# Kernel tuning notes

Measured on AMD Instinct MI355X. Metric: run time of the kernel, lower is better.

The kernel has to match this reference:

```python
import jax, jax.numpy as jnp
import numpy as np

B, D, E, H, L = 16384, 512, 16, 256, 64
NOISE_EPS = 0.01


def setup_inputs() -> dict:
    key = jax.random.key(0)
    ks = jax.random.split(key, 8)
    s = 0.05
    return {
        "x": jax.random.normal(ks[0], (B, D), dtype=jnp.float32),
        "noise": jax.random.normal(ks[1], (B, E), dtype=jnp.float32),
        "w_gate": jax.random.normal(ks[2], (D, E), dtype=jnp.float32) * s,
        "w_noise": jax.random.normal(ks[3], (D, E), dtype=jnp.float32) * s,
        "W1": jax.random.normal(ks[4], (E, D, H), dtype=jnp.float32) * s,
        "b1": jnp.zeros((E, H), dtype=jnp.float32),
        "W2": jax.random.normal(ks[5], (E, H, L), dtype=jnp.float32) * s,
        "b2": jnp.zeros((E, L), dtype=jnp.float32),
    }


def _noisy_gating(x, noise, w_gate, w_noise):
    clean_logits = x @ w_gate                                   # [B, E]
    noise_stddev = jax.nn.softplus(x @ w_noise) + NOISE_EPS     # [B, E]
    logits = jax.nn.softmax(clean_logits + noise * noise_stddev, axis=1)
    mean_weight = jnp.mean(logits, axis=-1) - 1e-8              # [B]
    gates = jnp.where(logits >= mean_weight[:, None], logits, 0.0)
    gates = gates / jnp.sum(gates, axis=-1, keepdims=True)
    return gates


def reference(x, noise, w_gate, w_noise, W1, b1, W2, b2):
    gates = _noisy_gating(x, noise, w_gate, w_noise)            # [B, E]
    # Dense equivalent of SparseDispatcher dispatch -> expert MLP -> combine:
    # combine scatters expert_e(x[b]) * gates[b,e] into slot (b, e), zeros elsewhere;
    # since gates==0 at masked slots, this equals gates[:,:,None] * all-expert outputs.
    h = jnp.tanh(jnp.einsum("bd,edh->beh", x, W1) + b1[None])   # [B, E, H]
    y = jnp.einsum("beh,ehl->bel", h, W2) + b2[None]            # [B, E, L]
    return gates[:, :, None] * y                                # [B, E, L]
```

## Files before the change

### kernel.cpp

```cpp
#include <hip/hip_runtime.h>
#include <stdint.h>

#define BROWS 16384
#define DDIM  512
#define EEXP  16
#define HDIM  256
#define LDIM  64
#define BM    64

typedef __bf16  bf16x8  __attribute__((ext_vector_type(8)));
typedef float   floatx4 __attribute__((ext_vector_type(4)));
typedef ushort  ushort8 __attribute__((ext_vector_type(8)));
typedef unsigned int u32;

__device__ __forceinline__ ushort f2bf(float f) {
    uint32_t u = __builtin_bit_cast(uint32_t, f);
    u += 0x7fffu + ((u >> 16) & 1u);
    return (ushort)(u >> 16);
}

__device__ __forceinline__ float fast_tanh(float x) {
    float e = __builtin_amdgcn_exp2f(x * 2.8853900817779268f);
    return 1.0f - 2.0f * __builtin_amdgcn_rcpf(e + 1.0f);
}

__device__ __forceinline__ void gl_lds16(const void* g, void* l) {
    __builtin_amdgcn_global_load_lds(
        (const __attribute__((address_space(1))) u32*)g,
        (__attribute__((address_space(3))) u32*)l, 16, 0, 0);
}

__global__ __launch_bounds__(256) void gate_aux_kernel(
    const float* __restrict__ x,
    const float* __restrict__ noise,
    const float* __restrict__ wg,
    const float* __restrict__ wn,
    const float* __restrict__ W1,
    const float* __restrict__ W2,
    float* __restrict__ gates,
    ushort* __restrict__ xbf,
    ushort* __restrict__ W1T,
    ushort* __restrict__ W2T,
    u32* __restrict__ cnt,
    u32* __restrict__ rowlist,
    float* __restrict__ out)
{
    if (blockIdx.x >= 512) {
        __shared__ float tile[32][33];
        int b = blockIdx.x - 512;
        const float* src; ushort* dst; int R, C, c0, r0, swz, ei;
        if (b < 2048) {
            ei = b >> 7; int rem = b & 127;
            c0 = (rem & 7) * 32; r0 = (rem >> 3) * 32;
            R = DDIM; C = HDIM; swz = 1;
            src = W1; dst = W1T;
        } else {
            b -= 2048;
            ei = b >> 4; int rem = b & 15;
            c0 = (rem & 1) * 32; r0 = (rem >> 1) * 32;
            R = HDIM; C = LDIM; swz = 0;
            src = W2; dst = W2T;
        }
        const int tx = threadIdx.x & 31, ty = threadIdx.x >> 5;
        const float* s = src + (size_t)ei * R * C;
        ushort* d = dst + (size_t)ei * R * C;

        #pragma unroll
        for (int i = 0; i < 4; ++i) {
            int rr = ty + i * 8;
            tile[rr][tx] = s[(size_t)(r0 + rr) * C + c0 + tx];
        }
        __syncthreads();
        #pragma unroll
        for (int i = 0; i < 4; ++i) {
            int cc = ty + i * 8;
            int h = c0 + cc;
            int col = r0 + tx;
            int col2 = col;
            if (swz) {
                int g = (col >> 3) & 7;
                col2 = (col & ~63) | ((g ^ (h & 7)) << 3) | (col & 7);
            }
            d[(size_t)h * R + col2] = f2bf(tile[tx][cc]);
        }
        return;
    }

    __shared__ __align__(16) float xs[32 * 132];
    __shared__ __align__(16) float wTg[16 * 132];
    __shared__ __align__(16) float wTn[16 * 132];
    __shared__ u32 lcnt[16];
    __shared__ u32 lbase[16];
    __shared__ ushort lrows[16 * 32];

    const int t    = threadIdx.x;
    const int blk  = blockIdx.x;
    const int row0 = blk * 32;
    const int og   = t & 15, rg = t >> 4;

    if (t < 16) lcnt[t] = 0;

    floatx4 accg4[2] = {}, accn4[2] = {};

    for (int ch = 0; ch < 4; ++ch) {
        const int k0 = ch * 128;
        __syncthreads();
        {
            int r = t >> 3, c = (t & 7) * 16;
            const float* src = &x[(size_t)(row0 + r) * DDIM + k0 + c];
            float4 f[4];
            #pragma unroll
            for (int i = 0; i < 4; ++i)
                f[i] = reinterpret_cast<const float4*>(src)[i];
            float* dst = &xs[r * 132 + c];
            #pragma unroll
            for (int i = 0; i < 4; ++i)
                reinterpret_cast<float4*>(dst)[i] = f[i];

            const int row = row0 + r;
            const int sw  = r & 7;
            #pragma unroll
            for (int i = 0; i < 2; ++i) {
                int cb = k0 + c + i * 8;
                int kb = cb >> 6;
                int g  = (cb >> 3) & 7;
                int gp = g ^ sw;
                float4 a = f[i * 2], b = f[i * 2 + 1];
                ushort8 t8;
                t8[0]=f2bf(a.x); t8[1]=f2bf(a.y); t8[2]=f2bf(a.z); t8[3]=f2bf(a.w);
                t8[4]=f2bf(b.x); t8[5]=f2bf(b.y); t8[6]=f2bf(b.z); t8[7]=f2bf(b.w);
                *reinterpret_cast<ushort8*>(&xbf[(size_t)row * DDIM + kb * 64 + gp * 8]) = t8;
            }
        }
        {
            int d = t >> 1, e0 = (t & 1) * 8;
            float4 a0 = *reinterpret_cast<const float4*>(&wg[(size_t)(k0 + d) * EEXP + e0]);
            float4 a1 = *reinterpret_cast<const float4*>(&wg[(size_t)(k0 + d) * EEXP + e0 + 4]);
            float4 b0 = *reinterpret_cast<const float4*>(&wn[(size_t)(k0 + d) * EEXP + e0]);
            float4 b1 = *reinterpret_cast<const float4*>(&wn[(size_t)(k0 + d) * EEXP + e0 + 4]);
            wTg[(e0+0)*132+d]=a0.x; wTg[(e0+1)*132+d]=a0.y; wTg[(e0+2)*132+d]=a0.z; wTg[(e0+3)*132+d]=a0.w;
            wTg[(e0+4)*132+d]=a1.x; wTg[(e0+5)*132+d]=a1.y; wTg[(e0+6)*132+d]=a1.z; wTg[(e0+7)*132+d]=a1.w;
            wTn[(e0+0)*132+d]=b0.x; wTn[(e0+1)*132+d]=b0.y; wTn[(e0+2)*132+d]=b0.z; wTn[(e0+3)*132+d]=b0.w;
            wTn[(e0+4)*132+d]=b1.x; wTn[(e0+5)*132+d]=b1.y; wTn[(e0+6)*132+d]=b1.z; wTn[(e0+7)*132+d]=b1.w;
        }
        __syncthreads();

        #pragma unroll 8
        for (int d4 = 0; d4 < 32; ++d4) {
            floatx4 wgv = *reinterpret_cast<const floatx4*>(&wTg[og * 132 + d4 * 4]);
            floatx4 wnv = *reinterpret_cast<const floatx4*>(&wTn[og * 132 + d4 * 4]);
            #pragma unroll
            for (int rr = 0; rr < 2; ++rr) {
                floatx4 xv = *reinterpret_cast<const floatx4*>(&xs[(rg * 2 + rr) * 132 + d4 * 4]);
                accg4[rr] += xv * wgv;
                accn4[rr] += xv * wnv;
            }
        }
    }

    #pragma unroll
    for (int rr = 0; rr < 2; ++rr) {
        const int row = row0 + rg * 2 + rr;
        float accg = accg4[rr][0] + accg4[rr][1] + accg4[rr][2] + accg4[rr][3];
        float accn = accn4[rr][0] + accn4[rr][1] + accn4[rr][2] + accn4[rr][3];

        float sp = fmaxf(accn, 0.f) + log1pf(expf(-fabsf(accn)));
        float stddev = sp + 0.01f;
        float nz = noise[(size_t)row * EEXP + og];
        float z = accg + nz * stddev;

        float m = z;
        #pragma unroll
        for (int mask = 8; mask >= 1; mask >>= 1)
            m = fmaxf(m, __shfl_xor(m, mask, 16));
        float ez = expf(z - m);
        float s = ez;
        #pragma unroll
        for (int mask = 8; mask >= 1; mask >>= 1)
            s += __shfl_xor(s, mask, 16);
        float logit = ez / s;

        float lsum = logit;
        #pragma unroll
        for (int mask = 8; mask >= 1; mask >>= 1)
            lsum += __shfl_xor(lsum, mask, 16);
        float mean = lsum * (1.0f / 16.0f) - 1e-8f;

        float gate = (logit >= mean) ? logit : 0.0f;
        float denom = gate;
        #pragma unroll
        for (int mask = 8; mask >= 1; mask >>= 1)
            denom += __shfl_xor(denom, mask, 16);

        gates[(size_t)row * EEXP + og] = gate / denom;

        if (gate > 0.0f) {
            u32 p = atomicAdd(&lcnt[og], 1u);
            lrows[og * 32 + p] = (ushort)(rg * 2 + rr);
        } else {
            float4 zf = {0.f, 0.f, 0.f, 0.f};
            float4* o = reinterpret_cast<float4*>(
                &out[(size_t)row * (EEXP * LDIM) + og * LDIM]);
            #pragma unroll
            for (int i = 0; i < 16; ++i) o[i] = zf;
        }
    }

    __syncthreads();
    if (t < 16) lbase[t] = atomicAdd(&cnt[t], lcnt[t]);
    __syncthreads();
    for (int i = t; i < 16 * 32; i += 256) {
        int e = i >> 5, j = i & 31;
        if ((u32)j < lcnt[e])
            rowlist[(size_t)e * BROWS + lbase[e] + j] = row0 + lrows[e * 32 + j];
    }
}

__global__ __launch_bounds__(256, 4) void expert_kernel(
    const ushort* __restrict__ xbf,
    const float*  __restrict__ gates,
    const ushort* __restrict__ W1T,
    const float*  __restrict__ b1,
    const ushort* __restrict__ W2T,
    const float*  __restrict__ b2,
    const u32*    __restrict__ cnt,
    const u32*    __restrict__ rowlist,
    float* __restrict__ out)
{
    __shared__ __align__(16) ushort lds[20480];

    const int bx = blockIdx.x;
    const int e  = bx & 15;
    const int t  = bx >> 4;

    const int count = (int)cnt[e];
    if (t * BM >= count) return;
    const int nrt = min(BM, count - t * BM);
    const u32* rl = rowlist + (size_t)e * BROWS + t * BM;

    const int tid  = threadIdx.x;
    const int lane = tid & 63;
    const int wave = tid >> 6;

    const int lr = lane & 15;
    const int q  = lane >> 4;
    const int kq = q * 8;
    const int rq = q * 4;
    const int la = lane >> 3, lb = lane & 7;

    const char* xg = (const char*)xbf;
    const char* w1 = (const char*)W1T + (size_t)e * HDIM * 1024;

    size_t abase[2]; int sxr[2];
    #pragma unroll
    for (int p = 0; p < 2; ++p) {
        int r  = wave * 16 + p * 8 + la;
        int rc = min(r, nrt - 1);
        u32 ri = rl[rc];
        abase[p] = (size_t)ri * 1024;
        sxr[p]   = (la ^ (int)(ri & 7)) << 4;
    }

    floatx4 acc[4][4] = {};

    for (int kb = 0; kb < 8; ++kb) {
        const int koff = kb * 128;
        #pragma unroll
        for (int p = 0; p < 2; ++p) {
            int c = wave * 2 + p;
            gl_lds16(xg + abase[p] + koff + ((lb << 4) ^ sxr[p]), &lds[c * 512]);
        }
        #pragma unroll
        for (int p = 0; p < 8; ++p) {
            int c = wave * 8 + p;
            gl_lds16(w1 + (size_t)(c * 8 + la) * 1024 + koff + (lb << 4),
                     &lds[4096 + c * 512]);
        }
        __syncthreads();

        #pragma unroll
        for (int s = 0; s < 2; ++s) {
            const int g = s * 4 + q;
            bf16x8 af[4], bfr[4];
            #pragma unroll
            for (int i = 0; i < 4; ++i) {
                int r = i * 16 + lr;
                af[i] = *reinterpret_cast<const bf16x8*>(&lds[r * 64 + ((g ^ (r & 7)) << 3)]);
            }
            #pragma unroll
            for (int j = 0; j < 4; ++j) {
                int r = wave * 64 + j * 16 + lr;
                bfr[j] = *reinterpret_cast<const bf16x8*>(&lds[4096 + r * 64 + ((g ^ (r & 7)) << 3)]);
            }
            #pragma unroll
            for (int i = 0; i < 4; ++i)
                #pragma unroll
                for (int j = 0; j < 4; ++j)
                    acc[i][j] = __builtin_amdgcn_mfma_f32_16x16x32_bf16(
                        af[i], bfr[j], acc[i][j], 0, 0, 0);
        }
        __syncthreads();
    }

    float b1v[4];
    #pragma unroll
    for (int j = 0; j < 4; ++j)
        b1v[j] = b1[e * HDIM + wave * 64 + j * 16 + lr];

    #pragma unroll
    for (int i = 0; i < 4; ++i)
        #pragma unroll
        for (int j = 0; j < 4; ++j) {
            int c = wave * 64 + j * 16 + lr;
            int gg = c >> 3;
            #pragma unroll
            for (int rr = 0; rr < 4; ++rr) {
                int r = i * 16 + rq + rr;
                float v = fast_tanh(acc[i][j][rr] + b1v[j]);
                lds[r * 256 + (((gg & 24) | ((gg & 7) ^ (r & 7))) << 3) + (c & 7)] = f2bf(v);
            }
        }
    __syncthreads();

    const ushort* w2 = W2T + (size_t)e * LDIM * HDIM;
    floatx4 acc2[4] = {};
    #pragma unroll
    for (int s = 0; s < 8; ++s) {
        int r = wave * 16 + lr;
        int g = s * 4 + q;
        bf16x8 af = *reinterpret_cast<const bf16x8*>(
            &lds[r * 256 + (((g & 24) | ((g & 7) ^ (r & 7))) << 3)]);
        #pragma unroll
        for (int j = 0; j < 4; ++j) {
            bf16x8 bfr = *reinterpret_cast<const bf16x8*>(
                &w2[(size_t)(j * 16 + lr) * HDIM + s * 32 + kq]);
            acc2[j] = __builtin_amdgcn_mfma_f32_16x16x32_bf16(af, bfr, acc2[j], 0, 0, 0);
        }
    }

    float b2v[4];
    #pragma unroll
    for (int j = 0; j < 4; ++j)
        b2v[j] = b2[e * LDIM + j * 16 + lr];

    #pragma unroll
    for (int rr = 0; rr < 4; ++rr) {
        int r  = wave * 16 + rq + rr;
        int rc = min(r, nrt - 1);
        u32 ri = rl[rc];
        float gsc = gates[(size_t)ri * EEXP + e];
        if (r < nrt) {
            #pragma unroll
            for (int j = 0; j < 4; ++j)
                out[(size_t)ri * (EEXP * LDIM) + e * LDIM + j * 16 + lr] =
                    (acc2[j][rr] + b2v[j]) * gsc;
        }
    }
}

extern "C" void kernel_launch(void* const* d_in, const int* in_sizes, int n_in,
                              void* d_out, int out_size, void* d_ws, size_t ws_size,
                              hipStream_t stream) {
    (void)in_sizes; (void)n_in; (void)out_size; (void)ws_size;
    const float* x     = (const float*)d_in[0];
    const float* noise = (const float*)d_in[1];
    const float* wg    = (const float*)d_in[2];
    const float* wn    = (const float*)d_in[3];
    const float* W1    = (const float*)d_in[4];
    const float* b1    = (const float*)d_in[5];
    const float* W2    = (const float*)d_in[6];
    const float* b2    = (const float*)d_in[7];
    float* out = (float*)d_out;

    char* ws = (char*)d_ws;
    float*  gates   = (float*)ws;
    ushort* W1T     = (ushort*)(ws + (1 << 20));
    ushort* W2T     = (ushort*)(ws + (5 << 20));
    ushort* xbf     = (ushort*)(ws + (6 << 20));
    u32*    cnt     = (u32*)(ws + (22 << 20));
    u32*    rowlist = (u32*)(ws + (24 << 20));

    hipMemsetAsync(cnt, 0, EEXP * sizeof(u32), stream);
    gate_aux_kernel<<<512 + 2304, 256, 0, stream>>>(
        x, noise, wg, wn, W1, W2, gates, xbf, W1T, W2T, cnt, rowlist, out);
    expert_kernel<<<(BROWS / BM) * EEXP, 256, 0, stream>>>(
        xbf, gates, W1T, b1, W2T, b2, cnt, rowlist, out);
}
```

Before: 177.2 us.

## Move zero-fill of masked output slots into idle expert-kernel blocks

Zero-filling of output slots whose gate is zero moves out of the gating kernel and into the expert kernel. Blocks that have no rows for their expert now pull 4096-float4 chunks from a global atomic counter and write zeros wherever the gate is zero. The goal is to take the scattered 256-byte stores off the gating kernel's critical path and use otherwise idle blocks to overlap them with expert compute. In exchange, every output element now costs a gates read, and idle blocks spin on an atomic work queue.

Result: slower. 211.4 us (+19.3%).

```diff
diff --git a/kernel.cpp b/kernel.cpp
--- a/kernel.cpp
+++ b/kernel.cpp
@@ -7,6 +7,7 @@
 #define HDIM  256
 #define LDIM  64
 #define BM    64
+#define ZCHUNKS 1024
 
 typedef __bf16  bf16x8  __attribute__((ext_vector_type(8)));
 typedef float   floatx4 __attribute__((ext_vector_type(4)));
@@ -42,8 +43,7 @@
     ushort* __restrict__ W1T,
     ushort* __restrict__ W2T,
     u32* __restrict__ cnt,
-    u32* __restrict__ rowlist,
-    float* __restrict__ out)
+    u32* __restrict__ rowlist)
 {
     if (blockIdx.x >= 512) {
         __shared__ float tile[32][33];
@@ -197,12 +197,6 @@
         if (gate > 0.0f) {
             u32 p = atomicAdd(&lcnt[og], 1u);
             lrows[og * 32 + p] = (ushort)(rg * 2 + rr);
-        } else {
-            float4 zf = {0.f, 0.f, 0.f, 0.f};
-            float4* o = reinterpret_cast<float4*>(
-                &out[(size_t)row * (EEXP * LDIM) + og * LDIM]);
-            #pragma unroll
-            for (int i = 0; i < 16; ++i) o[i] = zf;
         }
     }
 
@@ -224,6 +218,7 @@
     const ushort* __restrict__ W2T,
     const float*  __restrict__ b2,
     const u32*    __restrict__ cnt,
+    u32*          __restrict__ zfc,
     const u32*    __restrict__ rowlist,
     float* __restrict__ out)
 {
@@ -234,11 +229,33 @@
     const int t  = bx >> 4;
 
     const int count = (int)cnt[e];
-    if (t * BM >= count) return;
+    const int tid  = threadIdx.x;
+
+    if (t * BM >= count) {
+        __shared__ u32 chunk_s;
+        float4* o4 = reinterpret_cast<float4*>(out);
+        for (;;) {
+            if (tid == 0) chunk_s = atomicAdd(zfc, 1u);
+            __syncthreads();
+            u32 c = chunk_s;
+            __syncthreads();
+            if (c >= ZCHUNKS) return;
+            const u32 base = c * 4096;
+            #pragma unroll
+            for (int k = 0; k < 16; ++k) {
+                u32 idx = base + k * 256 + tid;
+                u32 slot = idx >> 4;
+                if (gates[slot] == 0.0f) {
+                    float4 z = {0.f, 0.f, 0.f, 0.f};
+                    o4[idx] = z;
+                }
+            }
+        }
+    }
+
     const int nrt = min(BM, count - t * BM);
     const u32* rl = rowlist + (size_t)e * BROWS + t * BM;
 
-    const int tid  = threadIdx.x;
     const int lane = tid & 63;
     const int wave = tid >> 6;
 
@@ -378,11 +395,12 @@
     ushort* W2T     = (ushort*)(ws + (5 << 20));
     ushort* xbf     = (ushort*)(ws + (6 << 20));
     u32*    cnt     = (u32*)(ws + (22 << 20));
+    u32*    zfc     = (u32*)(ws + (22 << 20) + 64);
     u32*    rowlist = (u32*)(ws + (24 << 20));
 
-    hipMemsetAsync(cnt, 0, EEXP * sizeof(u32), stream);
+    hipMemsetAsync(cnt, 0, 128, stream);
     gate_aux_kernel<<<512 + 2304, 256, 0, stream>>>(
-        x, noise, wg, wn, W1, W2, gates, xbf, W1T, W2T, cnt, rowlist, out);
+        x, noise, wg, wn, W1, W2, gates, xbf, W1T, W2T, cnt, rowlist);
     expert_kernel<<<(BROWS / BM) * EEXP, 256, 0, stream>>>(
-        xbf, gates, W1T, b1, W2T, b2, cnt, rowlist, out);
-}
+        xbf, gates, W1T, b1, W2T, b2, cnt, zfc, rowlist, out);
+}
```
